# Optimization experiments

Measured on AMD Instinct MI355X. Metric: run time of the kernel, lower is better.

## Reference

```python
import jax, jax.numpy as jnp
import numpy as np

NUM_BANDS = 8
NUM_CHANNELS = 16
KC = NUM_BANDS * NUM_CHANNELS
EMA_KERNEL_LENGTH = 100
DELTA = 0.1
EPS = 1e-06
S_INIT = 0.04


def setup_inputs() -> dict:
    key = jax.random.key(0)
    kx, = jax.random.split(key, 1)
    x = jax.random.normal(kx, (32, NUM_BANDS, NUM_CHANNELS, 8192), dtype=jnp.float32)
    alpha_raw = jnp.zeros((KC,), dtype=jnp.float32)
    log_s = jnp.full((KC,), float(np.log(S_INIT / (1.0 - S_INIT))), dtype=jnp.float32)
    return {"x": x, "alpha_raw": alpha_raw, "log_s": log_s}


def _build_ema_kernel(log_s):
    # (KC, 1, L_full) causal EMA kernel, then caller slices last L taps
    Lf = EMA_KERNEL_LENGTH
    s = jax.nn.sigmoid(log_s)                      # (KC,)
    j = jnp.arange(Lf, dtype=s.dtype)              # (Lf,)
    impulse = s[:, None] * (1.0 - s[:, None]) ** j[None, :]   # (KC, Lf)
    impulse = impulse / (impulse.sum(axis=1, keepdims=True) + 1e-08)
    kernel = impulse[:, ::-1]                      # flip to causal conv kernel
    return kernel[:, None, :]                      # (KC, 1, Lf)


def reference(x, alpha_raw, log_s):
    B, K, C, T = x.shape
    x_flat = x.reshape(B, KC, T)
    alpha = jax.nn.sigmoid(alpha_raw) * 0.5        # (KC,) in (0, 0.5)
    x_mag = jnp.abs(x_flat)
    L = min(EMA_KERNEL_LENGTH, T)
    kernel = _build_ema_kernel(log_s)[:, :, -L:]   # (KC, 1, L)
    x_padded = jnp.pad(x_mag, ((0, 0), (0, 0), (L - 1, 0)))
    # depthwise causal conv: groups = KC
    M = jax.lax.conv_general_dilated(
        x_padded, kernel,
        window_strides=(1,), padding='VALID',
        feature_group_count=KC,
        dimension_numbers=('NCH', 'OIH', 'NCH'))   # (B, KC, T)
    gain = jnp.clip(M, EPS, None) ** alpha[None, :, None] + DELTA
    out_flat = x_flat / gain
    return out_flat.reshape(B, K, C, T)
```

## Files before the change

kernel.cpp:

```cpp
#include <hip/hip_runtime.h>
#include <hip/hip_fp16.h>
#include <math.h>


constexpr int T      = 8192;
constexpr int KC_    = 128;
constexpr int LEN    = 100;
constexpr int BLOCK  = 256;
constexpr int CHUNK  = 32;
constexpr int PAD    = 104;
constexpr int TP     = T + PAD;
constexpr float EPS_   = 1e-6f;
constexpr float DELTA_ = 0.1f;
constexpr float LOG2E  = 1.4426950408889634f;

__device__ __forceinline__ int sk(int t) { return t + ((t >> 5) << 1); }

__device__ __forceinline__ float fast_sigmoid(float x) {
    const float e = __builtin_amdgcn_exp2f(-x * LOG2E);
    return __builtin_amdgcn_rcpf(1.0f + e);
}

__device__ __forceinline__ float gain_div(float xv, float M, float alpha) {
    const float Mc = fmaxf(M, EPS_);
    const float g  = __builtin_amdgcn_exp2f(alpha * __builtin_amdgcn_logf(Mc)) + DELTA_;
    return xv * __builtin_amdgcn_rcpf(g);
}

__global__ __launch_bounds__(BLOCK, 8) void agc_kernel(
    const float* __restrict__ x,
    const float* __restrict__ alpha_raw,
    const float* __restrict__ log_s,
    float* __restrict__ out)
{
    __shared__ __half lh[TP + ((TP >> 5) << 1)];
    __shared__ float  Pe[BLOCK + 3];

    const int row = blockIdx.x;
    const int kc  = row & (KC_ - 1);
    const int tid = threadIdx.x;
    const float* __restrict__ xrow = x + (size_t)row * T;
    float* __restrict__ orow       = out + (size_t)row * T;

    if (tid < PAD / 2)
        *reinterpret_cast<__half2*>(&lh[sk(2 * tid)]) =
            __float22half2_rn(make_float2(0.0f, 0.0f));
    if (tid < 3) Pe[tid] = 0.0f;

    #pragma unroll
    for (int it = 0; it < (T / 4) / BLOCK; ++it) {
        const int i = tid + it * BLOCK;
        const float4 v = reinterpret_cast<const float4*>(xrow)[i];
        const int e = sk(PAD + i * 4);
        *reinterpret_cast<__half2*>(&lh[e])     = __float22half2_rn(make_float2(v.x, v.y));
        *reinterpret_cast<__half2*>(&lh[e + 2]) = __float22half2_rn(make_float2(v.z, v.w));
    }

    const float s     = fast_sigmoid(log_s[kc]);
    const float alpha = 0.5f * fast_sigmoid(alpha_raw[kc]);
    const float q     = 1.0f - s;
    const float lq    = __builtin_amdgcn_logf(q);
    const float q32   = __builtin_amdgcn_exp2f(32.0f * lq);
    const float q64   = q32 * q32;
    const float q96   = q64 * q32;
    const float q100  = __builtin_amdgcn_exp2f(100.0f * lq);
    const float norm  = (1.0f - q100) + 1e-8f;
    const float w0    = s / norm;
    const float c3    = w0 * q100;

    __syncthreads();

    const int t0 = tid * CHUNK;

    auto ld2 = [&](int t) -> float2 {
        return __half22float2(*reinterpret_cast<const __half2*>(&lh[sk(PAD + t)]));
    };

    __half2 h2[CHUNK / 2];
    #pragma unroll
    for (int i = 0; i < CHUNK / 2; ++i)
        h2[i] = *reinterpret_cast<const __half2*>(&lh[sk(PAD + t0 + 2 * i)]);

    float P = 0.0f;
    const float qq = q * q;
    #pragma unroll
    for (int i = 0; i < CHUNK / 2; ++i) {
        const float2 f = __half22float2(h2[i]);
        P = fmaf(qq, P, fmaf(q, fabsf(f.x), fabsf(f.y)));
    }
    Pe[3 + tid] = P;
    __syncthreads();

    const float2 pA = ld2(t0 - 100);
    const float2 pB = ld2(t0 - 98);
    float corr = fmaf(q, fabsf(pA.x), fabsf(pA.y));
    corr = fmaf(q, corr, fabsf(pB.x));
    corr = fmaf(q, corr, fabsf(pB.y));
    float h = fmaf(q32, Pe[1 + tid], Pe[2 + tid]);
    h = fmaf(q64, Pe[tid], h);
    h = fmaf(q96, corr, h);
    float M = w0 * h;

    float o[4];
    #pragma unroll
    for (int m = 0; m < CHUNK / 2; ++m) {
        const float2 xf = __half22float2(h2[m]);
        const float2 xb = ld2(t0 - LEN + 2 * m);
        M = fmaf(q, M, fmaf(w0, fabsf(xf.x), -c3 * fabsf(xb.x)));
        o[(2 * m)     & 3] = gain_div(xf.x, M, alpha);
        M = fmaf(q, M, fmaf(w0, fabsf(xf.y), -c3 * fabsf(xb.y)));
        o[(2 * m + 1) & 3] = gain_div(xf.y, M, alpha);
        if (m & 1)
            reinterpret_cast<float4*>(orow)[(t0 >> 2) + (m >> 1)] =
                make_float4(o[0], o[1], o[2], o[3]);
    }
}

extern "C" void kernel_launch(void* const* d_in, const int* in_sizes, int n_in,
                              void* d_out, int out_size, void* d_ws, size_t ws_size,
                              hipStream_t stream) {
    const float* x         = (const float*)d_in[0];
    const float* alpha_raw = (const float*)d_in[1];
    const float* log_s     = (const float*)d_in[2];
    float* out             = (float*)d_out;
    const int nrows = in_sizes[0] / T;
    agc_kernel<<<nrows, BLOCK, 0, stream>>>(x, alpha_raw, log_s, out);
}
```

Before: 250.4 us.

## Split each row into four segments with halo, one float4 per thread

Each row is now processed by four blocks of 512 threads. Each block covers a 2048-sample segment and loads a 100-sample halo from the previous segment, instead of one block handling the whole row. Each thread handles four samples and rebuilds its EMA state by summing 25 preceding 4-sample partials from shared memory, replacing the three-term q32/q64/q96 combination. This raises grid parallelism and cuts per-block shared memory and register use, at the cost of extra halo reads and 25 FMAs of state setup per thread.

```diff
diff --git a/kernel.cpp b/kernel.cpp
--- a/kernel.cpp
+++ b/kernel.cpp
@@ -6,10 +6,13 @@
 constexpr int T      = 8192;
 constexpr int KC_    = 128;
 constexpr int LEN    = 100;
-constexpr int BLOCK  = 256;
-constexpr int CHUNK  = 32;
-constexpr int PAD    = 104;
-constexpr int TP     = T + PAD;
+constexpr int BLOCK  = 512;
+constexpr int CHUNK  = 4;
+constexpr int SEG    = BLOCK * CHUNK;
+constexpr int NSEG   = T / SEG;
+constexpr int PAD    = LEN;
+constexpr int NHALO  = PAD / CHUNK;
+constexpr int TP     = SEG + PAD;
 constexpr float EPS_   = 1e-6f;
 constexpr float DELTA_ = 0.1f;
 constexpr float LOG2E  = 1.4426950408889634f;
@@ -34,86 +37,82 @@
     float* __restrict__ out)
 {
     __shared__ __half lh[TP + ((TP >> 5) << 1)];
-    __shared__ float  Pe[BLOCK + 3];
+    __shared__ float  Pe[NHALO + BLOCK];
 
-    const int row = blockIdx.x;
+    const int bid = blockIdx.x;
+    const int row = bid >> 2;
+    const int seg = bid & (NSEG - 1);
+    const int g0  = seg * SEG;
     const int kc  = row & (KC_ - 1);
     const int tid = threadIdx.x;
     const float* __restrict__ xrow = x + (size_t)row * T;
     float* __restrict__ orow       = out + (size_t)row * T;
 
-    if (tid < PAD / 2)
-        *reinterpret_cast<__half2*>(&lh[sk(2 * tid)]) =
-            __float22half2_rn(make_float2(0.0f, 0.0f));
-    if (tid < 3) Pe[tid] = 0.0f;
-
-    #pragma unroll
-    for (int it = 0; it < (T / 4) / BLOCK; ++it) {
-        const int i = tid + it * BLOCK;
-        const float4 v = reinterpret_cast<const float4*>(xrow)[i];
-        const int e = sk(PAD + i * 4);
-        *reinterpret_cast<__half2*>(&lh[e])     = __float22half2_rn(make_float2(v.x, v.y));
-        *reinterpret_cast<__half2*>(&lh[e + 2]) = __float22half2_rn(make_float2(v.z, v.w));
-    }
-
     const float s     = fast_sigmoid(log_s[kc]);
     const float alpha = 0.5f * fast_sigmoid(alpha_raw[kc]);
     const float q     = 1.0f - s;
     const float lq    = __builtin_amdgcn_logf(q);
-    const float q32   = __builtin_amdgcn_exp2f(32.0f * lq);
-    const float q64   = q32 * q32;
-    const float q96   = q64 * q32;
+    const float qq    = q * q;
+    const float q4    = qq * qq;
     const float q100  = __builtin_amdgcn_exp2f(100.0f * lq);
     const float norm  = (1.0f - q100) + 1e-8f;
     const float w0    = s / norm;
     const float c3    = w0 * q100;
 
+    const int t0 = tid * CHUNK;
+
+    const float4 v = reinterpret_cast<const float4*>(xrow)[(g0 >> 2) + tid];
+    const __half2 ha = __float22half2_rn(make_float2(v.x, v.y));
+    const __half2 hb = __float22half2_rn(make_float2(v.z, v.w));
+    {
+        const int e = sk(PAD + t0);
+        *reinterpret_cast<__half2*>(&lh[e])     = ha;
+        *reinterpret_cast<__half2*>(&lh[e + 2]) = hb;
+    }
+    const float2 fA = __half22float2(ha);
+    const float2 fB = __half22float2(hb);
+    const float a0 = fabsf(fA.x), a1 = fabsf(fA.y);
+    const float a2 = fabsf(fB.x), a3 = fabsf(fB.y);
+    Pe[NHALO + tid] = fmaf(q, fmaf(q, fmaf(q, a0, a1), a2), a3);
+
+    if (tid < NHALO) {
+        float4 hv = make_float4(0.0f, 0.0f, 0.0f, 0.0f);
+        if (seg != 0)
+            hv = reinterpret_cast<const float4*>(xrow)[((g0 - PAD) >> 2) + tid];
+        const __half2 h0 = __float22half2_rn(make_float2(hv.x, hv.y));
+        const __half2 h1 = __float22half2_rn(make_float2(hv.z, hv.w));
+        const int e = sk(CHUNK * tid);
+        *reinterpret_cast<__half2*>(&lh[e])     = h0;
+        *reinterpret_cast<__half2*>(&lh[e + 2]) = h1;
+        const float2 f0 = __half22float2(h0);
+        const float2 f1 = __half22float2(h1);
+        Pe[tid] = fmaf(q, fmaf(q, fmaf(q, fabsf(f0.x), fabsf(f0.y)), fabsf(f1.x)),
+                       fabsf(f1.y));
+    }
+
     __syncthreads();
 
-    const int t0 = tid * CHUNK;
+    float acc = Pe[tid];
+    #pragma unroll
+    for (int i = 24; i >= 1; --i)
+        acc = fmaf(acc, q4, Pe[NHALO + tid - i]);
+    float M = w0 * acc;
 
-    auto ld2 = [&](int t) -> float2 {
-        return __half22float2(*reinterpret_cast<const __half2*>(&lh[sk(PAD + t)]));
-    };
+    const int eb = sk(t0);
+    const float2 tb0 = __half22float2(*reinterpret_cast<const __half2*>(&lh[eb]));
+    const float2 tb1 = __half22float2(*reinterpret_cast<const __half2*>(&lh[eb + 2]));
 
-    __half2 h2[CHUNK / 2];
-    #pragma unroll
-    for (int i = 0; i < CHUNK / 2; ++i)
-        h2[i] = *reinterpret_cast<const __half2*>(&lh[sk(PAD + t0 + 2 * i)]);
+    float4 o;
+    M = fmaf(q, M, fmaf(w0, a0, -c3 * fabsf(tb0.x)));
+    o.x = gain_div(fA.x, M, alpha);
+    M = fmaf(q, M, fmaf(w0, a1, -c3 * fabsf(tb0.y)));
+    o.y = gain_div(fA.y, M, alpha);
+    M = fmaf(q, M, fmaf(w0, a2, -c3 * fabsf(tb1.x)));
+    o.z = gain_div(fB.x, M, alpha);
+    M = fmaf(q, M, fmaf(w0, a3, -c3 * fabsf(tb1.y)));
+    o.w = gain_div(fB.y, M, alpha);
 
-    float P = 0.0f;
-    const float qq = q * q;
-    #pragma unroll
-    for (int i = 0; i < CHUNK / 2; ++i) {
-        const float2 f = __half22float2(h2[i]);
-        P = fmaf(qq, P, fmaf(q, fabsf(f.x), fabsf(f.y)));
-    }
-    Pe[3 + tid] = P;
-    __syncthreads();
-
-    const float2 pA = ld2(t0 - 100);
-    const float2 pB = ld2(t0 - 98);
-    float corr = fmaf(q, fabsf(pA.x), fabsf(pA.y));
-    corr = fmaf(q, corr, fabsf(pB.x));
-    corr = fmaf(q, corr, fabsf(pB.y));
-    float h = fmaf(q32, Pe[1 + tid], Pe[2 + tid]);
-    h = fmaf(q64, Pe[tid], h);
-    h = fmaf(q96, corr, h);
-    float M = w0 * h;
-
-    float o[4];
-    #pragma unroll
-    for (int m = 0; m < CHUNK / 2; ++m) {
-        const float2 xf = __half22float2(h2[m]);
-        const float2 xb = ld2(t0 - LEN + 2 * m);
-        M = fmaf(q, M, fmaf(w0, fabsf(xf.x), -c3 * fabsf(xb.x)));
-        o[(2 * m)     & 3] = gain_div(xf.x, M, alpha);
-        M = fmaf(q, M, fmaf(w0, fabsf(xf.y), -c3 * fabsf(xb.y)));
-        o[(2 * m + 1) & 3] = gain_div(xf.y, M, alpha);
-        if (m & 1)
-            reinterpret_cast<float4*>(orow)[(t0 >> 2) + (m >> 1)] =
-                make_float4(o[0], o[1], o[2], o[3]);
-    }
+    reinterpret_cast<float4*>(orow)[(g0 >> 2) + tid] = o;
 }
 
 extern "C" void kernel_launch(void* const* d_in, const int* in_sizes, int n_in,
@@ -124,5 +123,5 @@
     const float* log_s     = (const float*)d_in[2];
     float* out             = (float*)d_out;
     const int nrows = in_sizes[0] / T;
-    agc_kernel<<<nrows, BLOCK, 0, stream>>>(x, alpha_raw, log_s, out);
+    agc_kernel<<<nrows * NSEG, BLOCK, 0, stream>>>(x, alpha_raw, log_s, out);
 }
```

Result: faster. 227.6 us (-9.1%).
